# Kernel tuning notes

Measured on AMD Instinct MI355X. Metric: run time of the kernel, lower is better.

The kernel has to match this reference:

```python
import jax, jax.numpy as jnp
import numpy as np

N_NODES = 50000
N_EDGES = 600000
IN_DIM = 128
OUT_DIM = 128


def setup_inputs() -> dict:
    key = jax.random.key(0)
    k1, k2, k3, k4 = jax.random.split(key, 4)
    feature = jax.random.normal(k1, (N_NODES, IN_DIM), dtype=jnp.float32)
    W = jax.random.normal(k2, (IN_DIM, OUT_DIM), dtype=jnp.float32) * 0.05
    b = jnp.zeros((OUT_DIM,), dtype=jnp.float32)
    src = jax.random.randint(k3, (N_EDGES,), 0, N_NODES, dtype=jnp.int64 if jax.config.jax_enable_x64 else jnp.int32)
    dst = jax.random.randint(k4, (N_EDGES,), 0, N_NODES, dtype=jnp.int64 if jax.config.jax_enable_x64 else jnp.int32)
    return {"feature": feature, "W": W, "b": b, "src": src, "dst": dst}


def reference(feature, W, b, src, dst):
    # DGL GraphConv, norm='both' (eval mode => dropout is identity):
    #   out = relu( D_in^{-1/2} * A @ (D_out^{-1/2} * X) @ W + b )
    # degrees are clamped to a minimum of 1 as in DGL.
    n = feature.shape[0]
    ones = jnp.ones(src.shape[0], dtype=feature.dtype)
    out_deg = jnp.clip(jax.ops.segment_sum(ones, src, num_segments=n), 1.0)  # [N]
    in_deg = jnp.clip(jax.ops.segment_sum(ones, dst, num_segments=n), 1.0)   # [N]
    h = feature * jax.lax.rsqrt(out_deg)[:, None]                 # [N, in]
    agg = jax.ops.segment_sum(h[src], dst, num_segments=n)        # gather-scatter [N, in]
    agg = agg * jax.lax.rsqrt(in_deg)[:, None]
    out = agg @ W + b                                             # [N, out]
    return jax.nn.relu(out)
```

## Files before the change

### kernel.cpp

```cpp
#include <hip/hip_runtime.h>

constexpr int NODES = 50000;
constexpr int EDGES = 600000;
constexpr int DIM = 128;
constexpr int CHUNK = 1024;
constexpr int NB_SCAN = (NODES + CHUNK - 1) / CHUNK;
constexpr int HBINS = 8192;
constexpr int HRANGES = (NODES + HBINS - 1) / HBINS;
constexpr int HC = 40;
constexpr int EPC = EDGES / HC;
constexpr int EPC4 = EPC / 4;
constexpr int TW_BLOCKS = DIM * DIM / 256;

typedef __attribute__((ext_vector_type(8))) short short8v;
typedef __attribute__((ext_vector_type(8))) unsigned short ushort8v;
typedef __attribute__((ext_vector_type(4))) float f32x4;

__device__ __forceinline__ unsigned short f2bf(float f) {
    unsigned int b = __float_as_uint(f);
    b += 0x7fffu + ((b >> 16) & 1u);
    return (unsigned short)(b >> 16);
}

__device__ __forceinline__ int swz(int row, int oct) {
    return row * 256 + ((oct ^ (row & 7)) << 4);
}

__global__ __launch_bounds__(256) void prep_kernel(const float* __restrict__ W,
                                                   const int* __restrict__ src,
                                                   const int* __restrict__ dst,
                                                   unsigned short* __restrict__ Wt,
                                                   unsigned short* __restrict__ partial,
                                                   int* __restrict__ scan_part) {
    __shared__ int hs[HBINS];
    __shared__ int hd[HBINS];
    int b = blockIdx.x;
    int tid = threadIdx.x;
    if (b < TW_BLOCKS) {
        int t = b * 256 + tid;
        int n = t >> 7, k = t & 127;
        Wt[t] = f2bf(W[k * DIM + n]);
        if (b == 0 && tid < 64) scan_part[tid] = 0;
        return;
    }
    b -= TW_BLOCKS;
    int r = b / HC, c = b % HC;
    for (int i = tid; i < HBINS; i += 256) { hs[i] = 0; hd[i] = 0; }
    __syncthreads();
    const int4* s4 = reinterpret_cast<const int4*>(src);
    const int4* d4 = reinterpret_cast<const int4*>(dst);
    int t0 = c * EPC4;
    int base = r * HBINS;
    for (int t = t0 + tid; t < t0 + EPC4; t += 256) {
        int4 v = s4[t];
        int a;
        a = v.x - base; if ((unsigned)a < (unsigned)HBINS) atomicAdd(&hs[a], 1);
        a = v.y - base; if ((unsigned)a < (unsigned)HBINS) atomicAdd(&hs[a], 1);
        a = v.z - base; if ((unsigned)a < (unsigned)HBINS) atomicAdd(&hs[a], 1);
        a = v.w - base; if ((unsigned)a < (unsigned)HBINS) atomicAdd(&hs[a], 1);
        int4 w = d4[t];
        a = w.x - base; if ((unsigned)a < (unsigned)HBINS) atomicAdd(&hd[a], 1);
        a = w.y - base; if ((unsigned)a < (unsigned)HBINS) atomicAdd(&hd[a], 1);
        a = w.z - base; if ((unsigned)a < (unsigned)HBINS) atomicAdd(&hd[a], 1);
        a = w.w - base; if ((unsigned)a < (unsigned)HBINS) atomicAdd(&hd[a], 1);
    }
    __syncthreads();
    unsigned short* ops = partial + (size_t)(r * HC + c) * HBINS;
    unsigned short* opd = ops + (size_t)HRANGES * HC * HBINS;
    for (int i = tid; i < HBINS; i += 256) {
        ops[i] = (unsigned short)hs[i];
        opd[i] = (unsigned short)hd[i];
    }
}

__global__ __launch_bounds__(256) void deg_coff(const unsigned short* __restrict__ partial,
                                                int* __restrict__ deg_out,
                                                int* __restrict__ deg_in,
                                                unsigned short* __restrict__ cumoff,
                                                int* __restrict__ scan_part) {
    __shared__ int bsum[4];
    int tid = threadIdx.x;
    int n = blockIdx.x * 256 + tid;
    int r = n >> 13, bin = n & (HBINS - 1);
    const unsigned short* ps = partial;
    const unsigned short* pd = partial + (size_t)HRANGES * HC * HBINS;
    int s0 = 0, run = 0;
    #pragma unroll 8
    for (int c = 0; c < HC; ++c) {
        size_t idx = (size_t)(r * HC + c) * HBINS + bin;
        s0 += ps[idx];
        cumoff[idx] = (unsigned short)run;
        run += pd[idx];
    }
    if (n < NODES) {
        deg_out[n] = s0;
        deg_in[n] = run;
    }
    int lane = tid & 63, wid = tid >> 6;
    int v = (n < NODES) ? run : 0;
    #pragma unroll
    for (int off = 32; off; off >>= 1) v += __shfl_down(v, off, 64);
    if (lane == 0) bsum[wid] = v;
    __syncthreads();
    if (tid == 0)
        atomicAdd(&scan_part[blockIdx.x >> 2], bsum[0] + bsum[1] + bsum[2] + bsum[3]);
}

__global__ __launch_bounds__(256) void scan_chunks(const int* __restrict__ deg_in,
                                                   const int* __restrict__ scan_part,
                                                   int* __restrict__ row_start) {
    __shared__ int wsum[4];
    __shared__ int blockoff_s;
    int b = blockIdx.x, tid = threadIdx.x, lane = tid & 63, wid = tid >> 6;
    if (wid == 0) {
        int v = (lane < b) ? scan_part[lane] : 0;
        #pragma unroll
        for (int off = 32; off; off >>= 1) v += __shfl_down(v, off, 64);
        if (lane == 0) blockoff_s = v;
    }
    int base = b * CHUNK + tid * 4;
    int v[4];
    int s = 0;
    #pragma unroll
    for (int i = 0; i < 4; ++i) {
        v[i] = (base + i < NODES) ? deg_in[base + i] : 0;
        s += v[i];
    }
    int incl = s;
    #pragma unroll
    for (int off = 1; off < 64; off <<= 1) {
        int t = __shfl_up(incl, off, 64);
        if (lane >= off) incl += t;
    }
    if (lane == 63) wsum[wid] = incl;
    __syncthreads();
    int wbase = 0;
    for (int w = 0; w < wid; ++w) wbase += wsum[w];
    int run = blockoff_s + wbase + incl - s;
    #pragma unroll
    for (int i = 0; i < 4; ++i) {
        if (base + i < NODES) row_start[base + i] = run;
        run += v[i];
    }
}

__global__ __launch_bounds__(256) void bucket_lds(const int* __restrict__ src,
                                                  const int* __restrict__ dst,
                                                  const int* __restrict__ row_start,
                                                  const unsigned short* __restrict__ cumoff,
                                                  int* __restrict__ csr_src) {
    __shared__ int cur[HBINS];
    int r = blockIdx.x / HC, c = blockIdx.x % HC;
    int tid = threadIdx.x;
    int base = r * HBINS;
    const unsigned short* co = cumoff + (size_t)(r * HC + c) * HBINS;
    for (int i = tid; i < HBINS; i += 256) {
        int n = base + i;
        int rs = (n < NODES) ? row_start[n] : 0;
        cur[i] = rs + (int)co[i];
    }
    __syncthreads();
    const int4* dst4 = reinterpret_cast<const int4*>(dst);
    const int4* src4 = reinterpret_cast<const int4*>(src);
    int t0 = c * EPC4;
    for (int t = t0 + tid; t < t0 + EPC4; t += 256) {
        int4 dv = dst4[t];
        int4 sv = src4[t];
        int d;
        d = dv.x - base; if ((unsigned)d < (unsigned)HBINS) csr_src[atomicAdd(&cur[d], 1)] = sv.x;
        d = dv.y - base; if ((unsigned)d < (unsigned)HBINS) csr_src[atomicAdd(&cur[d], 1)] = sv.y;
        d = dv.z - base; if ((unsigned)d < (unsigned)HBINS) csr_src[atomicAdd(&cur[d], 1)] = sv.z;
        d = dv.w - base; if ((unsigned)d < (unsigned)HBINS) csr_src[atomicAdd(&cur[d], 1)] = sv.w;
    }
}

__global__ __launch_bounds__(256) void gemm_mfma(const float* __restrict__ X,
                                                 const int* __restrict__ deg_out,
                                                 const unsigned short* __restrict__ Wt,
                                                 unsigned short* __restrict__ H) {
    __shared__ char XsB[64 * 256];
    __shared__ char WsB[128 * 256];
    int tid = threadIdx.x;
    int row0 = blockIdx.x * 64;

    for (int t = tid; t < 128 * 16; t += 256) {
        int n = t >> 4, o = t & 15;
        ushort8v wv = *reinterpret_cast<const ushort8v*>(Wt + n * DIM + o * 8);
        *reinterpret_cast<ushort8v*>(WsB + swz(n, o)) = wv;
    }
    for (int t = tid; t < 64 * 16; t += 256) {
        int r = t >> 4, o = t & 15;
        int node = row0 + r;
        float4 v0 = make_float4(0.f, 0.f, 0.f, 0.f), v1 = v0;
        float sc = 0.f;
        if (node < NODES) {
            const float4* rp = reinterpret_cast<const float4*>(X + (size_t)node * DIM);
            v0 = rp[o * 2];
            v1 = rp[o * 2 + 1];
            int dg = deg_out[node];
            sc = rsqrtf((float)(dg > 0 ? dg : 1));
        }
        ushort8v h;
        h[0] = f2bf(v0.x * sc); h[1] = f2bf(v0.y * sc);
        h[2] = f2bf(v0.z * sc); h[3] = f2bf(v0.w * sc);
        h[4] = f2bf(v1.x * sc); h[5] = f2bf(v1.y * sc);
        h[6] = f2bf(v1.z * sc); h[7] = f2bf(v1.w * sc);
        *reinterpret_cast<ushort8v*>(XsB + swz(r, o)) = h;
    }
    __syncthreads();

    int w = tid >> 6, l = tid & 63;
    int lr = l & 15, lg = l >> 4;
    f32x4 acc[8];
    #pragma unroll
    for (int nt = 0; nt < 8; ++nt) acc[nt] = (f32x4){0.f, 0.f, 0.f, 0.f};
    #pragma unroll
    for (int kb = 0; kb < 4; ++kb) {
        short8v a = *reinterpret_cast<short8v*>(XsB + swz(w * 16 + lr, kb * 4 + lg));
        #pragma unroll
        for (int nt = 0; nt < 8; ++nt) {
            short8v bfr = *reinterpret_cast<short8v*>(WsB + swz(nt * 16 + lr, kb * 4 + lg));
            acc[nt] = __builtin_amdgcn_mfma_f32_16x16x32_bf16(a, bfr, acc[nt], 0, 0, 0);
        }
    }
    #pragma unroll
    for (int nt = 0; nt < 8; ++nt) {
        int col = nt * 16 + lr;
        #pragma unroll
        for (int rg = 0; rg < 4; ++rg) {
            int m = w * 16 + lg * 4 + rg;
            int byte = m * 256 + (((col >> 3) ^ (m & 7)) << 4) + (col & 7) * 2;
            *reinterpret_cast<unsigned short*>(XsB + byte) = f2bf(acc[nt][rg]);
        }
    }
    __syncthreads();
    for (int t = tid; t < 64 * 16; t += 256) {
        int r = t >> 4, o = t & 15;
        int node = row0 + r;
        if (node < NODES)
            *reinterpret_cast<ushort8v*>(H + (size_t)node * DIM + o * 8) =
                *reinterpret_cast<ushort8v*>(XsB + swz(r, o));
    }
}

__global__ __launch_bounds__(256) void gather_kernel(const uint2* __restrict__ H2,
                                                     const int* __restrict__ row_start,
                                                     const int* __restrict__ deg_in,
                                                     const int* __restrict__ csr_src,
                                                     const float* __restrict__ bias,
                                                     float* __restrict__ out) {
    int gw = (blockIdx.x * 256 + threadIdx.x) >> 6;
    int lane = threadIdx.x & 63;
    if (gw >= NODES) return;
    int half = lane >> 5;
    int sub = lane & 31;
    int start = row_start[gw];
    int deg = deg_in[gw];
    float ax = 0.f, ay = 0.f, az = 0.f, aw = 0.f;
    for (int i0 = 0; i0 < deg; i0 += 64) {
        int nv = min(64, deg - i0);
        int sv = 0;
        if (i0 + lane < deg) sv = csr_src[start + i0 + lane];
        int i = 0;
        for (; i + 8 <= nv; i += 8) {
            int s0 = __shfl(sv, i + half, 64);
            int s1 = __shfl(sv, i + 2 + half, 64);
            int s2 = __shfl(sv, i + 4 + half, 64);
            int s3 = __shfl(sv, i + 6 + half, 64);
            uint2 u0 = H2[(size_t)s0 * 32 + sub];
            uint2 u1 = H2[(size_t)s1 * 32 + sub];
            uint2 u2 = H2[(size_t)s2 * 32 + sub];
            uint2 u3 = H2[(size_t)s3 * 32 + sub];
            ax += __uint_as_float(u0.x << 16); ay += __uint_as_float(u0.x & 0xffff0000u);
            az += __uint_as_float(u0.y << 16); aw += __uint_as_float(u0.y & 0xffff0000u);
            ax += __uint_as_float(u1.x << 16); ay += __uint_as_float(u1.x & 0xffff0000u);
            az += __uint_as_float(u1.y << 16); aw += __uint_as_float(u1.y & 0xffff0000u);
            ax += __uint_as_float(u2.x << 16); ay += __uint_as_float(u2.x & 0xffff0000u);
            az += __uint_as_float(u2.y << 16); aw += __uint_as_float(u2.y & 0xffff0000u);
            ax += __uint_as_float(u3.x << 16); ay += __uint_as_float(u3.x & 0xffff0000u);
            az += __uint_as_float(u3.y << 16); aw += __uint_as_float(u3.y & 0xffff0000u);
        }
        for (; i + 2 <= nv; i += 2) {
            int s = __shfl(sv, i + half, 64);
            uint2 u = H2[(size_t)s * 32 + sub];
            ax += __uint_as_float(u.x << 16); ay += __uint_as_float(u.x & 0xffff0000u);
            az += __uint_as_float(u.y << 16); aw += __uint_as_float(u.y & 0xffff0000u);
        }
        if (i < nv) {
            int s = __shfl(sv, i, 64);
            if (half == 0) {
                uint2 u = H2[(size_t)s * 32 + sub];
                ax += __uint_as_float(u.x << 16); ay += __uint_as_float(u.x & 0xffff0000u);
                az += __uint_as_float(u.y << 16); aw += __uint_as_float(u.y & 0xffff0000u);
            }
        }
    }
    ax += __shfl_xor(ax, 32, 64);
    ay += __shfl_xor(ay, 32, 64);
    az += __shfl_xor(az, 32, 64);
    aw += __shfl_xor(aw, 32, 64);
    if (half == 0) {
        float sc = rsqrtf((float)(deg > 0 ? deg : 1));
        float4 bb = reinterpret_cast<const float4*>(bias)[sub];
        float4 o;
        o.x = fmaxf(ax * sc + bb.x, 0.f);
        o.y = fmaxf(ay * sc + bb.y, 0.f);
        o.z = fmaxf(az * sc + bb.z, 0.f);
        o.w = fmaxf(aw * sc + bb.w, 0.f);
        reinterpret_cast<float4*>(out)[(size_t)gw * 32 + sub] = o;
    }
}

extern "C" void kernel_launch(void* const* d_in, const int* in_sizes, int n_in,
                              void* d_out, int out_size, void* d_ws, size_t ws_size,
                              hipStream_t stream) {
    const float* feat = (const float*)d_in[0];
    const float* W    = (const float*)d_in[1];
    const float* b    = (const float*)d_in[2];
    const int*   src  = (const int*)d_in[3];
    const int*   dst  = (const int*)d_in[4];
    float* out = (float*)d_out;

    constexpr size_t PART_ELEMS = (size_t)HRANGES * HC * HBINS;

    char* p = (char*)d_ws;
    unsigned short* partial = (unsigned short*)p;
    unsigned short* cumoff  = partial + 2 * PART_ELEMS;
    unsigned short* H       = (unsigned short*)p;
    p += 3 * PART_ELEMS * sizeof(unsigned short);
    unsigned short* Wt = (unsigned short*)p;  p += (size_t)DIM * DIM * 2;
    int* deg_out   = (int*)p;  p += (size_t)NODES * 4;
    int* deg_in    = (int*)p;  p += (size_t)NODES * 4;
    int* row_start = (int*)p;  p += (size_t)NODES * 4;
    int* scan_part = (int*)p;  p += 256;
    int* csr_src   = (int*)p;

    prep_kernel<<<TW_BLOCKS + HRANGES * HC, 256, 0, stream>>>(W, src, dst, Wt, partial, scan_part);
    deg_coff<<<(HRANGES * HBINS) / 256, 256, 0, stream>>>(partial, deg_out, deg_in, cumoff, scan_part);
    scan_chunks<<<NB_SCAN, 256, 0, stream>>>(deg_in, scan_part, row_start);
    bucket_lds<<<HRANGES * HC, 256, 0, stream>>>(src, dst, row_start, cumoff, csr_src);
    gemm_mfma<<<(NODES + 63) / 64, 256, 0, stream>>>(feat, deg_out, Wt, H);
    gather_kernel<<<(NODES * 64 + 255) / 256, 256, 0, stream>>>(
        (const uint2*)H, row_start, deg_in, csr_src, b, out);
}
```

Before: 166.6 us.

## Pack histogram bins as 16-bit pairs and split src/dst histogram blocks

Histogram and bucketing counters are now packed two 16-bit counts per 32-bit LDS word, which lets each block cover 32768 nodes. Node ranges drop from 7 to 2, so each block scans the edge list far fewer times. Src and dst histograms move to separate blocks, with the dst side split into 80 chunks, and bucket_lds now reads row_start per edge instead of folding it into the LDS cursor. This cuts redundant edge reads across ranges, at the cost of a scattered global row_start read per edge and a risk of 16-bit overflow if a per-chunk count exceeds 65535.

```diff
diff --git a/kernel.cpp b/kernel.cpp
--- a/kernel.cpp
+++ b/kernel.cpp
@@ -5,11 +5,13 @@
 constexpr int DIM = 128;
 constexpr int CHUNK = 1024;
 constexpr int NB_SCAN = (NODES + CHUNK - 1) / CHUNK;
-constexpr int HBINS = 8192;
-constexpr int HRANGES = (NODES + HBINS - 1) / HBINS;
-constexpr int HC = 40;
-constexpr int EPC = EDGES / HC;
-constexpr int EPC4 = EPC / 4;
+constexpr int HB = 32768;
+constexpr int HB2 = HB / 2;
+constexpr int NR = 2;
+constexpr int HCS = 40;
+constexpr int EPCS4 = EDGES / HCS / 4;
+constexpr int HCD = 80;
+constexpr int EPCD4 = EDGES / HCD / 4;
 constexpr int TW_BLOCKS = DIM * DIM / 256;
 
 typedef __attribute__((ext_vector_type(8))) short short8v;
@@ -30,50 +32,51 @@
                                                    const int* __restrict__ src,
                                                    const int* __restrict__ dst,
                                                    unsigned short* __restrict__ Wt,
-                                                   unsigned short* __restrict__ partial,
+                                                   unsigned short* __restrict__ part_s,
+                                                   unsigned short* __restrict__ part_d,
                                                    int* __restrict__ scan_part) {
-    __shared__ int hs[HBINS];
-    __shared__ int hd[HBINS];
-    int b = blockIdx.x;
-    int tid = threadIdx.x;
+    __shared__ unsigned int h[HB2];
+    int b = blockIdx.x, tid = threadIdx.x;
     if (b < TW_BLOCKS) {
         int t = b * 256 + tid;
-        int n = t >> 7, k = t & 127;
-        Wt[t] = f2bf(W[k * DIM + n]);
+        Wt[t] = f2bf(W[(t & 127) * DIM + (t >> 7)]);
         if (b == 0 && tid < 64) scan_part[tid] = 0;
         return;
     }
     b -= TW_BLOCKS;
-    int r = b / HC, c = b % HC;
-    for (int i = tid; i < HBINS; i += 256) { hs[i] = 0; hd[i] = 0; }
-    __syncthreads();
-    const int4* s4 = reinterpret_cast<const int4*>(src);
-    const int4* d4 = reinterpret_cast<const int4*>(dst);
-    int t0 = c * EPC4;
-    int base = r * HBINS;
-    for (int t = t0 + tid; t < t0 + EPC4; t += 256) {
-        int4 v = s4[t];
+    const int4* e4;
+    int r, nb4, t0;
+    unsigned short* outp;
+    if (b < NR * HCS) {
+        r = b / HCS;
+        e4 = reinterpret_cast<const int4*>(src);
+        nb4 = EPCS4; t0 = (b % HCS) * EPCS4;
+        outp = part_s + (size_t)b * HB;
+    } else {
+        b -= NR * HCS;
+        r = b / HCD;
+        e4 = reinterpret_cast<const int4*>(dst);
+        nb4 = EPCD4; t0 = (b % HCD) * EPCD4;
+        outp = part_d + (size_t)b * HB;
+    }
+    for (int i = tid; i < HB2; i += 256) h[i] = 0;
+    __syncthreads();
+    int base = r * HB;
+    for (int t = t0 + tid; t < t0 + nb4; t += 256) {
+        int4 v = e4[t];
         int a;
-        a = v.x - base; if ((unsigned)a < (unsigned)HBINS) atomicAdd(&hs[a], 1);
-        a = v.y - base; if ((unsigned)a < (unsigned)HBINS) atomicAdd(&hs[a], 1);
-        a = v.z - base; if ((unsigned)a < (unsigned)HBINS) atomicAdd(&hs[a], 1);
-        a = v.w - base; if ((unsigned)a < (unsigned)HBINS) atomicAdd(&hs[a], 1);
-        int4 w = d4[t];
-        a = w.x - base; if ((unsigned)a < (unsigned)HBINS) atomicAdd(&hd[a], 1);
-        a = w.y - base; if ((unsigned)a < (unsigned)HBINS) atomicAdd(&hd[a], 1);
-        a = w.z - base; if ((unsigned)a < (unsigned)HBINS) atomicAdd(&hd[a], 1);
-        a = w.w - base; if ((unsigned)a < (unsigned)HBINS) atomicAdd(&hd[a], 1);
-    }
-    __syncthreads();
-    unsigned short* ops = partial + (size_t)(r * HC + c) * HBINS;
-    unsigned short* opd = ops + (size_t)HRANGES * HC * HBINS;
-    for (int i = tid; i < HBINS; i += 256) {
-        ops[i] = (unsigned short)hs[i];
-        opd[i] = (unsigned short)hd[i];
-    }
-}
-
-__global__ __launch_bounds__(256) void deg_coff(const unsigned short* __restrict__ partial,
+        a = v.x - base; if ((unsigned)a < (unsigned)HB) atomicAdd(&h[a >> 1], 1u << (16 * (a & 1)));
+        a = v.y - base; if ((unsigned)a < (unsigned)HB) atomicAdd(&h[a >> 1], 1u << (16 * (a & 1)));
+        a = v.z - base; if ((unsigned)a < (unsigned)HB) atomicAdd(&h[a >> 1], 1u << (16 * (a & 1)));
+        a = v.w - base; if ((unsigned)a < (unsigned)HB) atomicAdd(&h[a >> 1], 1u << (16 * (a & 1)));
+    }
+    __syncthreads();
+    unsigned int* o32 = reinterpret_cast<unsigned int*>(outp);
+    for (int i = tid; i < HB2; i += 256) o32[i] = h[i];
+}
+
+__global__ __launch_bounds__(256) void deg_coff(const unsigned short* __restrict__ part_s,
+                                                const unsigned short* __restrict__ part_d,
                                                 int* __restrict__ deg_out,
                                                 int* __restrict__ deg_in,
                                                 unsigned short* __restrict__ cumoff,
@@ -81,16 +84,17 @@
     __shared__ int bsum[4];
     int tid = threadIdx.x;
     int n = blockIdx.x * 256 + tid;
-    int r = n >> 13, bin = n & (HBINS - 1);
-    const unsigned short* ps = partial;
-    const unsigned short* pd = partial + (size_t)HRANGES * HC * HBINS;
-    int s0 = 0, run = 0;
+    int r = n >> 15, bin = n & (HB - 1);
+    int s0 = 0;
     #pragma unroll 8
-    for (int c = 0; c < HC; ++c) {
-        size_t idx = (size_t)(r * HC + c) * HBINS + bin;
-        s0 += ps[idx];
+    for (int c = 0; c < HCS; ++c)
+        s0 += part_s[(size_t)(r * HCS + c) * HB + bin];
+    int run = 0;
+    #pragma unroll 8
+    for (int c = 0; c < HCD; ++c) {
+        size_t idx = (size_t)(r * HCD + c) * HB + bin;
         cumoff[idx] = (unsigned short)run;
-        run += pd[idx];
+        run += part_d[idx];
     }
     if (n < NODES) {
         deg_out[n] = s0;
@@ -149,28 +153,42 @@
                                                   const int* __restrict__ row_start,
                                                   const unsigned short* __restrict__ cumoff,
                                                   int* __restrict__ csr_src) {
-    __shared__ int cur[HBINS];
-    int r = blockIdx.x / HC, c = blockIdx.x % HC;
+    __shared__ unsigned int cur[HB2];
+    int b = blockIdx.x;
+    int r = b / HCD, c = b % HCD;
     int tid = threadIdx.x;
-    int base = r * HBINS;
-    const unsigned short* co = cumoff + (size_t)(r * HC + c) * HBINS;
-    for (int i = tid; i < HBINS; i += 256) {
-        int n = base + i;
-        int rs = (n < NODES) ? row_start[n] : 0;
-        cur[i] = rs + (int)co[i];
-    }
-    __syncthreads();
-    const int4* dst4 = reinterpret_cast<const int4*>(dst);
-    const int4* src4 = reinterpret_cast<const int4*>(src);
-    int t0 = c * EPC4;
-    for (int t = t0 + tid; t < t0 + EPC4; t += 256) {
-        int4 dv = dst4[t];
-        int4 sv = src4[t];
+    int base = r * HB;
+    const unsigned int* co32 = reinterpret_cast<const unsigned int*>(cumoff + (size_t)b * HB);
+    for (int i = tid; i < HB2; i += 256) cur[i] = co32[i];
+    __syncthreads();
+    const int4* d4 = reinterpret_cast<const int4*>(dst);
+    const int4* s4 = reinterpret_cast<const int4*>(src);
+    int t0 = c * EPCD4;
+    for (int t = t0 + tid; t < t0 + EPCD4; t += 256) {
+        int4 dv = d4[t];
+        int4 sv = s4[t];
         int d;
-        d = dv.x - base; if ((unsigned)d < (unsigned)HBINS) csr_src[atomicAdd(&cur[d], 1)] = sv.x;
-        d = dv.y - base; if ((unsigned)d < (unsigned)HBINS) csr_src[atomicAdd(&cur[d], 1)] = sv.y;
-        d = dv.z - base; if ((unsigned)d < (unsigned)HBINS) csr_src[atomicAdd(&cur[d], 1)] = sv.z;
-        d = dv.w - base; if ((unsigned)d < (unsigned)HBINS) csr_src[atomicAdd(&cur[d], 1)] = sv.w;
+        unsigned int old;
+        d = dv.x - base;
+        if ((unsigned)d < (unsigned)HB) {
+            old = atomicAdd(&cur[d >> 1], 1u << (16 * (d & 1)));
+            csr_src[row_start[base + d] + ((old >> (16 * (d & 1))) & 0xffff)] = sv.x;
+        }
+        d = dv.y - base;
+        if ((unsigned)d < (unsigned)HB) {
+            old = atomicAdd(&cur[d >> 1], 1u << (16 * (d & 1)));
+            csr_src[row_start[base + d] + ((old >> (16 * (d & 1))) & 0xffff)] = sv.y;
+        }
+        d = dv.z - base;
+        if ((unsigned)d < (unsigned)HB) {
+            old = atomicAdd(&cur[d >> 1], 1u << (16 * (d & 1)));
+            csr_src[row_start[base + d] + ((old >> (16 * (d & 1))) & 0xffff)] = sv.z;
+        }
+        d = dv.w - base;
+        if ((unsigned)d < (unsigned)HB) {
+            old = atomicAdd(&cur[d >> 1], 1u << (16 * (d & 1)));
+            csr_src[row_start[base + d] + ((old >> (16 * (d & 1))) & 0xffff)] = sv.w;
+        }
     }
 }
 
@@ -321,13 +339,15 @@
     const int*   dst  = (const int*)d_in[4];
     float* out = (float*)d_out;
 
-    constexpr size_t PART_ELEMS = (size_t)HRANGES * HC * HBINS;
+    constexpr size_t PART_S_ELEMS = (size_t)NR * HCS * HB;
+    constexpr size_t PART_D_ELEMS = (size_t)NR * HCD * HB;
 
     char* p = (char*)d_ws;
-    unsigned short* partial = (unsigned short*)p;
-    unsigned short* cumoff  = partial + 2 * PART_ELEMS;
-    unsigned short* H       = (unsigned short*)p;
-    p += 3 * PART_ELEMS * sizeof(unsigned short);
+    unsigned short* part_s = (unsigned short*)p;
+    unsigned short* part_d = part_s + PART_S_ELEMS;
+    unsigned short* cumoff = part_d + PART_D_ELEMS;
+    unsigned short* H      = (unsigned short*)p;
+    p += (PART_S_ELEMS + 2 * PART_D_ELEMS) * sizeof(unsigned short);
     unsigned short* Wt = (unsigned short*)p;  p += (size_t)DIM * DIM * 2;
     int* deg_out   = (int*)p;  p += (size_t)NODES * 4;
     int* deg_in    = (int*)p;  p += (size_t)NODES * 4;
@@ -335,10 +355,12 @@
     int* scan_part = (int*)p;  p += 256;
     int* csr_src   = (int*)p;
 
-    prep_kernel<<<TW_BLOCKS + HRANGES * HC, 256, 0, stream>>>(W, src, dst, Wt, partial, scan_part);
-    deg_coff<<<(HRANGES * HBINS) / 256, 256, 0, stream>>>(partial, deg_out, deg_in, cumoff, scan_part);
+    prep_kernel<<<TW_BLOCKS + NR * HCS + NR * HCD, 256, 0, stream>>>(
+        W, src, dst, Wt, part_s, part_d, scan_part);
+    deg_coff<<<(NR * HB) / 256, 256, 0, stream>>>(
+        part_s, part_d, deg_out, deg_in, cumoff, scan_part);
     scan_chunks<<<NB_SCAN, 256, 0, stream>>>(deg_in, scan_part, row_start);
-    bucket_lds<<<HRANGES * HC, 256, 0, stream>>>(src, dst, row_start, cumoff, csr_src);
+    bucket_lds<<<NR * HCD, 256, 0, stream>>>(src, dst, row_start, cumoff, csr_src);
     gemm_mfma<<<(NODES + 63) / 64, 256, 0, stream>>>(feat, deg_out, Wt, H);
     gather_kernel<<<(NODES * 64 + 255) / 256, 256, 0, stream>>>(
         (const uint2*)H, row_start, deg_in, csr_src, b, out);
```

After: 155.4 us. 6.7% less time.
